# Kernel tuning notes

Hardware: AMD Instinct MI355X
Metric: run time of the kernel (lower is better)

Reference implementation:

```python
import jax, jax.numpy as jnp
import numpy as np

EPS = 1e-12  # torch F.normalize default eps

def l2norm(x, axis):
    n = jnp.sqrt(jnp.sum(x * x, axis=axis, keepdims=True))
    return x / jnp.maximum(n, EPS)

def conv2d(x, w, b, pad):
    y = jax.lax.conv_general_dilated(x, w, (1, 1), [(pad, pad), (pad, pad)],
                                     dimension_numbers=('NCHW', 'OIHW', 'NCHW'))
    return y + b[None, :, None, None]

def setup_inputs() -> dict:
    key = jax.random.key(0)
    ks = jax.random.split(key, 12)
    N, C, H, W, K = 16, 256, 64, 64, 32
    s = 0.05
    return {
        'feature':   jax.random.normal(ks[0], (N, C, H, W), jnp.float32),
        'conv_up_w': jax.random.normal(ks[1], (K, C, 3, 3), jnp.float32) * s,
        'conv_up_b': jax.random.normal(ks[2], (K,), jnp.float32) * s,
        'centroids': jax.random.uniform(ks[3], (K, C), jnp.float32),
        'upfc_w':    jax.random.normal(ks[4], (C, K * C), jnp.float32) * s,
        'upfc_b':    jax.random.normal(ks[5], (C,), jnp.float32) * s,
        't1_w':      jax.random.normal(ks[6], (C, 2 * C, 1, 1), jnp.float32) * s,
        't1_b':      jax.random.normal(ks[7], (C,), jnp.float32) * s,
        't2_w':      jax.random.normal(ks[8], (C, C, 1, 1), jnp.float32) * s,
        't2_b':      jax.random.normal(ks[9], (C,), jnp.float32) * s,
    }

def reference(feature, conv_up_w, conv_up_b, centroids, upfc_w, upfc_b, t1_w, t1_b, t2_w, t2_b):
    N, C, H, W = feature.shape
    K = centroids.shape[0]
    # --- UP branch ---
    xn = l2norm(feature, axis=1)                       # (N,C,H,W)
    sa = jax.nn.softmax(conv2d(xn, conv_up_w, conv_up_b, 1), axis=1)  # (N,K,H,W)
    sa_flat = sa.reshape(N, K, H * W)                  # (N,K,L)
    x_flat = xn.reshape(N, C, H * W)                   # (N,C,L)
    # sum_l sa[n,k,l] * (x[n,c,l] - centroid[k,c])  ==  two matmuls, no (N,K,C,L) tensor
    up = jnp.einsum('nkl,ncl->nkc', sa_flat, x_flat) \
         - jnp.sum(sa_flat, axis=-1)[:, :, None] * centroids[None]   # (N,K,C)
    up = l2norm(up, axis=2).reshape(N, K * C)
    up = l2norm(up, axis=1)
    up = up @ upfc_w.T + upfc_b                        # (N,C)
    up_map = jnp.broadcast_to(up[:, :, None, None], (N, C, H, W))
    # --- transform ---
    nf = jnp.concatenate([feature, up_map], axis=1)    # (N,2C,H,W)
    h = jax.nn.relu(conv2d(nf, t1_w, t1_b, 0))
    return jax.nn.relu(conv2d(h, t2_w, t2_b, 0))
```

## Files before the change

### kernel.cpp

```cpp
#include <hip/hip_runtime.h>
#include <cstdint>

#define N_ 16
#define C_ 256
#define H_ 64
#define W_ 64
#define L_ 4096
#define K_ 32
#define CL_ (C_*L_)
#define KL_ (K_*L_)
#define KC_ (K_*C_)

typedef __attribute__((ext_vector_type(8))) short short8;
typedef __attribute__((ext_vector_type(4))) float f32x4;

__device__ __forceinline__ unsigned short f2bf(float x) {
    unsigned int u = __float_as_uint(x);
    u += 0x7fffu + ((u >> 16) & 1u);
    return (unsigned short)(u >> 16);
}
__device__ __forceinline__ unsigned int pack2(float a, float b) {
    return (unsigned int)f2bf(a) | ((unsigned int)f2bf(b) << 16);
}

__global__ __launch_bounds__(256) void k_prep(
    const float* __restrict__ f, float* __restrict__ rinv,
    unsigned short* __restrict__ xnb)
{
    __shared__ float tile[256 * 34];
    __shared__ float ssred[8 * 33];
    __shared__ float rbuf[32];
    int bid = blockIdx.x;
    int n = bid >> 7;
    int l0 = (bid & 127) << 5;
    int tid = threadIdx.x;
    int l = tid & 31, cb = tid >> 5;
    const float* fp = f + (size_t)n * CL_ + l0 + l;
    float ss = 0.f;
#pragma unroll
    for (int i = 0; i < 32; ++i) {
        int c = (cb << 5) + i;
        float v = fp[(size_t)c * L_];
        tile[c * 34 + l] = v;
        ss = fmaf(v, v, ss);
    }
    ssred[cb * 33 + l] = ss;
    __syncthreads();
    if (tid < 32) {
        float s = 0.f;
#pragma unroll
        for (int j = 0; j < 8; ++j) s += ssred[j * 33 + tid];
        float ri = 1.0f / fmaxf(sqrtf(s), 1e-12f);
        rinv[n * L_ + l0 + tid] = ri;
        rbuf[tid] = ri;
    }
    __syncthreads();
    float ri = rbuf[l];
    unsigned short* op = xnb + ((size_t)n * L_ + l0 + l) * C_ + (cb << 5);
#pragma unroll
    for (int g = 0; g < 4; ++g) {
        unsigned int pk[4];
#pragma unroll
        for (int d = 0; d < 4; ++d) {
            int c = (cb << 5) + (g << 3) + (d << 1);
            pk[d] = pack2(tile[c * 34 + l] * ri, tile[(c + 1) * 34 + l] * ri);
        }
        *(uint4*)(op + (g << 3)) = make_uint4(pk[0], pk[1], pk[2], pk[3]);
    }
}

__global__ __launch_bounds__(256) void k_wpack(const float* __restrict__ w, unsigned short* __restrict__ wb) {
    int i = blockIdx.x * 256 + threadIdx.x;
    int j = i & 7;
    int k = (i >> 3) & 31;
    int q = (i >> 8) & 3;
    int ch = (i >> 10) & 7;
    int t = i >> 13;
    int c = (ch << 5) + (q << 3) + j;
    wb[i] = f2bf(w[k * 2304 + c * 9 + t]);
}

__global__ __launch_bounds__(256) void k_wpack2(const float* __restrict__ w, int stride,
                                                unsigned short* __restrict__ wb) {
    int i = blockIdx.x * 256 + threadIdx.x;
    int co = i >> 8, ci = i & 255;
    wb[i] = f2bf(w[(size_t)co * stride + ci]);
}

__global__ __launch_bounds__(128, 2) void k_conv(
    const unsigned short* __restrict__ xnb, const unsigned short* __restrict__ wb,
    const float* __restrict__ bias, float* __restrict__ sa, float* __restrict__ ssum)
{
    __shared__ __align__(16) unsigned short lsB[2][3 * 34 * 40];
    __shared__ float sred[2][32];
    int bid = blockIdx.x;
    int n = bid & 15, y = (bid >> 4) & 63, px_b = bid >> 10;
    int tid = threadIdx.x;
    int wv = tid >> 6, lane = tid & 63;
    int r = lane & 15, quad = lane >> 4;
    int pxw = (wv << 4) + r;
    int xbase = (px_b << 5) - 1;
    const unsigned short* xb = xnb + (size_t)n * CL_;

    const unsigned short* sptr[4];
    int sidx[4];
    bool svalid[4];
    int scnt = (tid < 24) ? 4 : 3;
#pragma unroll
    for (int k = 0; k < 4; ++k) {
        int j = tid + (k << 7);
        int row = j / 136; if (row > 2) row = 2;
        int rem = j - row * 136;
        int px = rem >> 2, q = rem & 3;
        int yy = y + row - 1, xx = xbase + px;
        bool ok = ((unsigned)yy < 64u) && ((unsigned)xx < 64u);
        int yc = ok ? yy : 0, xc = ok ? xx : 0;
        sptr[k] = xb + (((size_t)(yc << 6) + xc) << 8) + (q << 3);
        svalid[k] = ok;
        sidx[k] = (row * 34 + px) * 40 + (q << 3);
    }
    const uint4 z4 = make_uint4(0, 0, 0, 0);
    uint4 pre[4];
#pragma unroll
    for (int k = 0; k < 4; ++k)
        pre[k] = (k < scnt && svalid[k]) ? *(const uint4*)sptr[k] : z4;

    const unsigned short* wlane = wb + (quad << 8) + (r << 3);

    f32x4 acc0 = (f32x4){0.f, 0.f, 0.f, 0.f};
    f32x4 acc1 = (f32x4){0.f, 0.f, 0.f, 0.f};
    for (int i = 0; i < 8; ++i) {
        int c0 = i << 5;
        unsigned short* buf = lsB[i & 1];
#pragma unroll
        for (int k = 0; k < 4; ++k)
            if (k < scnt) *(uint4*)(buf + sidx[k]) = pre[k];
        __syncthreads();
        if (i < 7) {
#pragma unroll
            for (int k = 0; k < 4; ++k)
                pre[k] = (k < scnt && svalid[k]) ? *(const uint4*)(sptr[k] + c0 + 32) : z4;
        }
#pragma unroll
        for (int dy = 0; dy < 3; ++dy) {
            short8 A0r[3], A1r[3], Br[3];
#pragma unroll
            for (int dx = 0; dx < 3; ++dx) {
                int t = dy * 3 + dx;
                const unsigned short* wp = wlane + (((t << 3) + i) << 10);
                A0r[dx] = *(const short8*)wp;
                A1r[dx] = *(const short8*)(wp + 128);
                Br[dx]  = *(const short8*)(buf + (dy * 34 + pxw + dx) * 40 + (quad << 3));
            }
#pragma unroll
            for (int dx = 0; dx < 3; ++dx) {
                acc0 = __builtin_amdgcn_mfma_f32_16x16x32_bf16(A0r[dx], Br[dx], acc0, 0, 0, 0);
                acc1 = __builtin_amdgcn_mfma_f32_16x16x32_bf16(A1r[dx], Br[dx], acc1, 0, 0, 0);
            }
        }
    }
    float4 b0 = *(const float4*)(bias + (quad << 2));
    float4 b1 = *(const float4*)(bias + 16 + (quad << 2));
    float v[8];
    v[0] = acc0[0] + b0.x; v[1] = acc0[1] + b0.y; v[2] = acc0[2] + b0.z; v[3] = acc0[3] + b0.w;
    v[4] = acc1[0] + b1.x; v[5] = acc1[1] + b1.y; v[6] = acc1[2] + b1.z; v[7] = acc1[3] + b1.w;
    float mx = v[0];
#pragma unroll
    for (int j = 1; j < 8; ++j) mx = fmaxf(mx, v[j]);
    mx = fmaxf(mx, __shfl_xor(mx, 16));
    mx = fmaxf(mx, __shfl_xor(mx, 32));
    float s = 0.f;
#pragma unroll
    for (int j = 0; j < 8; ++j) { v[j] = __expf(v[j] - mx); s += v[j]; }
    s += __shfl_xor(s, 16);
    s += __shfl_xor(s, 32);
    float rs = 1.0f / s;
    float sv8[8];
#pragma unroll
    for (int j = 0; j < 8; ++j) sv8[j] = v[j] * rs;
    int l = (y << 6) + (px_b << 5) + pxw;
    float* sp = sa + (size_t)n * KL_ + l;
#pragma unroll
    for (int j = 0; j < 4; ++j) {
        sp[(size_t)((quad << 2) + j) * L_] = sv8[j];
        sp[(size_t)(16 + (quad << 2) + j) * L_] = sv8[4 + j];
    }
#pragma unroll
    for (int j = 0; j < 8; ++j) {
        float a = sv8[j];
        a += __shfl_xor(a, 1); a += __shfl_xor(a, 2);
        a += __shfl_xor(a, 4); a += __shfl_xor(a, 8);
        sv8[j] = a;
    }
    if (r == 0) {
#pragma unroll
        for (int j = 0; j < 4; ++j) {
            sred[wv][(quad << 2) + j] = sv8[j];
            sred[wv][16 + (quad << 2) + j] = sv8[4 + j];
        }
    }
    __syncthreads();
    if (tid < 32) {
        float t = sred[0][tid] + sred[1][tid];
        atomicAdd(ssum + n * K_ + tid, t);
    }
}

__global__ __launch_bounds__(256) void k_einsum(
    const float* __restrict__ f, const float* __restrict__ rinv,
    const float* __restrict__ sa, float* __restrict__ up)
{
    __shared__ float xn_s[C_ * 33];
    __shared__ float sa_s[K_ * 32];
    int bid = blockIdx.x;
    int n = bid >> 5;
    int l0 = (bid & 31) << 7;
    int tid = threadIdx.x;
    int kq = tid >> 5, cq = tid & 31;
    float acc[4][8];
#pragma unroll
    for (int i = 0; i < 4; ++i)
#pragma unroll
        for (int j = 0; j < 8; ++j) acc[i][j] = 0.f;

    for (int ch = 0; ch < 4; ++ch) {
        int lc = l0 + (ch << 5);
        __syncthreads();
        {
            int crow = tid >> 3, lq = (tid & 7) << 2;
#pragma unroll
            for (int p = 0; p < 8; ++p) {
                int c = (p << 5) + crow;
                float4 f4 = *(const float4*)(f + (size_t)n * CL_ + (size_t)c * L_ + lc + lq);
                float4 r4 = *(const float4*)(rinv + n * L_ + lc + lq);
                float* d = xn_s + c * 33 + lq;
                d[0] = f4.x * r4.x; d[1] = f4.y * r4.y; d[2] = f4.z * r4.z; d[3] = f4.w * r4.w;
            }
        }
        {
            int k = tid >> 3, lq = (tid & 7) << 2;
            float4 a4 = *(const float4*)(sa + (size_t)n * KL_ + (size_t)k * L_ + lc + lq);
            *(float4*)(sa_s + (k << 5) + lq) = a4;
        }
        __syncthreads();
#pragma unroll 4
        for (int l = 0; l < 32; ++l) {
            float sv[4], xv[8];
#pragma unroll
            for (int i = 0; i < 4; ++i) sv[i] = sa_s[((kq << 2) + i) * 32 + l];
#pragma unroll
            for (int j = 0; j < 8; ++j) xv[j] = xn_s[(cq + (j << 5)) * 33 + l];
#pragma unroll
            for (int i = 0; i < 4; ++i)
#pragma unroll
                for (int j = 0; j < 8; ++j) acc[i][j] = fmaf(sv[i], xv[j], acc[i][j]);
        }
    }
    float* upp = up + (size_t)n * KC_;
#pragma unroll
    for (int i = 0; i < 4; ++i)
#pragma unroll
        for (int j = 0; j < 8; ++j)
            atomicAdd(upp + ((kq << 2) + i) * C_ + cq + (j << 5), acc[i][j]);
}

__global__ __launch_bounds__(256) void k_rowfix(
    const float* __restrict__ up, const float* __restrict__ ssum,
    const float* __restrict__ cent, float* __restrict__ upn, float* __restrict__ rowss)
{
    __shared__ float red[256];
    int bid = blockIdx.x;
    int k = bid & 31;
    float sv = ssum[bid];
    float v = up[(size_t)bid * C_ + threadIdx.x] - sv * cent[k * C_ + threadIdx.x];
    red[threadIdx.x] = v * v; __syncthreads();
    for (int st = 128; st > 0; st >>= 1) {
        if (threadIdx.x < st) red[threadIdx.x] += red[threadIdx.x + st];
        __syncthreads();
    }
    float ss = red[0];
    float ri = 1.0f / fmaxf(sqrtf(ss), 1e-12f);
    upn[(size_t)bid * C_ + threadIdx.x] = v * ri;
    if (threadIdx.x == 0) rowss[bid] = ss * ri * ri;
}

__global__ __launch_bounds__(256) void k_fc(
    const float* __restrict__ upn, const float* __restrict__ rowss,
    const float* __restrict__ w, const float* __restrict__ b,
    float* __restrict__ upvec)
{
    __shared__ float rnb[16];
    __shared__ float red[16][5];
    int c = blockIdx.x;
    int tid = threadIdx.x;
    int wv = tid >> 6, lane = tid & 63;
    if (tid < 16) {
        float ts = 0.f;
#pragma unroll
        for (int k = 0; k < K_; ++k) ts += rowss[(tid << 5) + k];
        rnb[tid] = 1.0f / fmaxf(sqrtf(ts), 1e-12f);
    }
    float acc[16];
#pragma unroll
    for (int n = 0; n < 16; ++n) acc[n] = 0.f;
    const float* wr = w + (size_t)c * KC_;
#pragma unroll
    for (int g = 0; g < 8; ++g) {
        int kc = (g << 10) + (tid << 2);
        float4 w4 = *(const float4*)(wr + kc);
#pragma unroll
        for (int n = 0; n < 16; ++n) {
            float4 u4 = *(const float4*)(upn + n * KC_ + kc);
            acc[n] += w4.x * u4.x + w4.y * u4.y + w4.z * u4.z + w4.w * u4.w;
        }
    }
#pragma unroll
    for (int n = 0; n < 16; ++n) {
        float a = acc[n];
#pragma unroll
        for (int s = 1; s < 64; s <<= 1) a += __shfl_xor(a, s);
        if (lane == 0) red[n][wv] = a;
    }
    __syncthreads();
    if (tid < 16) {
        float v = red[tid][0] + red[tid][1] + red[tid][2] + red[tid][3];
        upvec[tid * C_ + c] = v * rnb[tid] + b[c];
    }
}

__global__ __launch_bounds__(256) void k_t1up(
    const float* __restrict__ upvec, const float* __restrict__ t1w,
    const float* __restrict__ t1b, float* __restrict__ t1up)
{
    __shared__ float wld[256];
    int co = blockIdx.x;
    int tid = threadIdx.x;
    wld[tid] = t1w[(size_t)co * 512 + 256 + tid];
    __syncthreads();
    int n = tid >> 4, s = tid & 15;
    float a = 0.f;
#pragma unroll
    for (int i = 0; i < 16; ++i)
        a += wld[s + (i << 4)] * upvec[n * C_ + s + (i << 4)];
#pragma unroll
    for (int st = 1; st < 16; st <<= 1) a += __shfl_xor(a, st);
    if (s == 0) t1up[n * C_ + co] = a + t1b[co];
}

__global__ __launch_bounds__(256) void k_gemm1(
    const float* __restrict__ f, const unsigned short* __restrict__ wb,
    const float* __restrict__ t1up, unsigned short* __restrict__ hb)
{
    __shared__ __align__(16) unsigned int lsB[2][128 * 20];
    int bid = blockIdx.x;
    int co_b = bid & 1, px_b = (bid >> 1) & 31, n = bid >> 6;
    int l0 = px_b << 7;
    int tid = threadIdx.x;
    int wv = tid >> 6, lane = tid & 63;
    int r = lane & 15, quad = lane >> 4;
    int pxl = (wv >> 1) << 6;
    int co0 = (co_b << 7) + ((wv & 1) << 6);
    const float* fb_ = f + (size_t)n * CL_ + l0;
    int c2 = tid & 15, pxg = tid >> 4;

    unsigned int pk[2][4];
#pragma unroll
    for (int k2 = 0; k2 < 2; ++k2) {
        const float* s0 = fb_ + (size_t)(c2 << 1) * L_ + ((pxg + (k2 << 4)) << 2);
        float4 a = *(const float4*)s0;
        float4 b = *(const float4*)(s0 + L_);
        pk[k2][0] = pack2(a.x, b.x); pk[k2][1] = pack2(a.y, b.y);
        pk[k2][2] = pack2(a.z, b.z); pk[k2][3] = pack2(a.w, b.w);
    }
    f32x4 acc[4][4];
#pragma unroll
    for (int i = 0; i < 4; ++i)
#pragma unroll
        for (int j = 0; j < 4; ++j) acc[i][j] = (f32x4){0.f, 0.f, 0.f, 0.f};

    for (int i = 0; i < 8; ++i) {
        int c0 = i << 5;
        unsigned int* buf = lsB[i & 1];
#pragma unroll
        for (int k2 = 0; k2 < 2; ++k2) {
            int base = (pxg + (k2 << 4)) * 80 + c2;
            buf[base]      = pk[k2][0];
            buf[base + 20] = pk[k2][1];
            buf[base + 40] = pk[k2][2];
            buf[base + 60] = pk[k2][3];
        }
        __syncthreads();
        if (i < 7) {
#pragma unroll
            for (int k2 = 0; k2 < 2; ++k2) {
                const float* s0 = fb_ + (size_t)(c0 + 32 + (c2 << 1)) * L_ + ((pxg + (k2 << 4)) << 2);
                float4 a = *(const float4*)s0;
                float4 b = *(const float4*)(s0 + L_);
                pk[k2][0] = pack2(a.x, b.x); pk[k2][1] = pack2(a.y, b.y);
                pk[k2][2] = pack2(a.z, b.z); pk[k2][3] = pack2(a.w, b.w);
            }
        }
        short8 A[4], B[4];
#pragma unroll
        for (int t = 0; t < 4; ++t)
            A[t] = *(const short8*)(wb + (size_t)(co0 + (t << 4) + r) * C_ + c0 + (quad << 3));
#pragma unroll
        for (int t = 0; t < 4; ++t)
            B[t] = *(const short8*)((const unsigned short*)buf + (pxl + (t << 4) + r) * 40 + (quad << 3));
#pragma unroll
        for (int pxt = 0; pxt < 4; ++pxt)
#pragma unroll
            for (int cot = 0; cot < 4; ++cot)
                acc[pxt][cot] = __builtin_amdgcn_mfma_f32_16x16x32_bf16(A[cot], B[pxt], acc[pxt][cot], 0, 0, 0);
    }
#pragma unroll
    for (int pxt = 0; pxt < 4; ++pxt) {
        int px = l0 + pxl + (pxt << 4) + r;
        unsigned short* orow = hb + ((size_t)n * L_ + px) * C_;
#pragma unroll
        for (int cot = 0; cot < 4; ++cot) {
            int cb = co0 + (cot << 4) + (quad << 2);
            float4 bb = *(const float4*)(t1up + n * C_ + cb);
            unsigned int p0 = pack2(fmaxf(acc[pxt][cot][0] + bb.x, 0.f),
                                    fmaxf(acc[pxt][cot][1] + bb.y, 0.f));
            unsigned int p1 = pack2(fmaxf(acc[pxt][cot][2] + bb.z, 0.f),
                                    fmaxf(acc[pxt][cot][3] + bb.w, 0.f));
            *(uint2*)(orow + cb) = make_uint2(p0, p1);
        }
    }
}

__global__ __launch_bounds__(256) void k_gemm2(
    const unsigned short* __restrict__ hb, const unsigned short* __restrict__ wb,
    const float* __restrict__ t2b, float* __restrict__ out)
{
    __shared__ __align__(16) unsigned short lsB[2][128 * 40];
    int bid = blockIdx.x;
    int co_b = bid & 1, px_b = (bid >> 1) & 31, n = bid >> 6;
    int l0 = px_b << 7;
    int tid = threadIdx.x;
    int wv = tid >> 6, lane = tid & 63;
    int r = lane & 15, quad = lane >> 4;
    int pxl = (wv >> 1) << 6;
    int co0 = (co_b << 7) + ((wv & 1) << 6);
    const unsigned short* hrow = hb + ((size_t)n * L_ + l0) * C_;
    int q = tid & 3, pxs = tid >> 2;

    uint4 pre[2];
#pragma unroll
    for (int k2 = 0; k2 < 2; ++k2)
        pre[k2] = *(const uint4*)(hrow + (size_t)(pxs + (k2 << 6)) * C_ + (q << 3));

    f32x4 acc[4][4];
#pragma unroll
    for (int i = 0; i < 4; ++i)
#pragma unroll
        for (int j = 0; j < 4; ++j) acc[i][j] = (f32x4){0.f, 0.f, 0.f, 0.f};

    for (int i = 0; i < 8; ++i) {
        int c0 = i << 5;
        unsigned short* buf = lsB[i & 1];
#pragma unroll
        for (int k2 = 0; k2 < 2; ++k2)
            *(uint4*)(buf + (pxs + (k2 << 6)) * 40 + (q << 3)) = pre[k2];
        __syncthreads();
        if (i < 7) {
#pragma unroll
            for (int k2 = 0; k2 < 2; ++k2)
                pre[k2] = *(const uint4*)(hrow + (size_t)(pxs + (k2 << 6)) * C_ + c0 + 32 + (q << 3));
        }
        short8 A[4], B[4];
#pragma unroll
        for (int t = 0; t < 4; ++t)
            A[t] = *(const short8*)(wb + (size_t)(co0 + (t << 4) + r) * C_ + c0 + (quad << 3));
#pragma unroll
        for (int t = 0; t < 4; ++t)
            B[t] = *(const short8*)(buf + (pxl + (t << 4) + r) * 40 + (quad << 3));
#pragma unroll
        for (int pxt = 0; pxt < 4; ++pxt)
#pragma unroll
            for (int cot = 0; cot < 4; ++cot)
                acc[pxt][cot] = __builtin_amdgcn_mfma_f32_16x16x32_bf16(A[cot], B[pxt], acc[pxt][cot], 0, 0, 0);
    }
#pragma unroll
    for (int pxt = 0; pxt < 4; ++pxt) {
        int px = l0 + pxl + (pxt << 4) + r;
#pragma unroll
        for (int cot = 0; cot < 4; ++cot) {
            int cb = co0 + (cot << 4) + (quad << 2);
            float4 bb = *(const float4*)(t2b + cb);
            out[((size_t)n * C_ + cb + 0) * L_ + px] = fmaxf(acc[pxt][cot][0] + bb.x, 0.f);
            out[((size_t)n * C_ + cb + 1) * L_ + px] = fmaxf(acc[pxt][cot][1] + bb.y, 0.f);
            out[((size_t)n * C_ + cb + 2) * L_ + px] = fmaxf(acc[pxt][cot][2] + bb.z, 0.f);
            out[((size_t)n * C_ + cb + 3) * L_ + px] = fmaxf(acc[pxt][cot][3] + bb.w, 0.f);
        }
    }
}

extern "C" void kernel_launch(void* const* d_in, const int* in_sizes, int n_in,
                              void* d_out, int out_size, void* d_ws, size_t ws_size,
                              hipStream_t stream)
{
    const float* feature = (const float*)d_in[0];
    const float* conv_w  = (const float*)d_in[1];
    const float* conv_b  = (const float*)d_in[2];
    const float* cent    = (const float*)d_in[3];
    const float* upfc_w  = (const float*)d_in[4];
    const float* upfc_b  = (const float*)d_in[5];
    const float* t1w     = (const float*)d_in[6];
    const float* t1b     = (const float*)d_in[7];
    const float* t2w     = (const float*)d_in[8];
    const float* t2b     = (const float*)d_in[9];

    float* ws = (float*)d_ws;
    unsigned short* xnb = (unsigned short*)ws;
    unsigned short* hb  = xnb;
    float* rest  = ws + 8388608;
    float* rinv  = rest;
    float* sa    = rinv + 65536;
    float* up    = sa + 2097152;
    float* ssum  = up + 131072;
    float* upn   = ssum + 512;
    float* rowss = upn + 131072;
    float* upvec = rowss + 512;
    float* t1up  = upvec + 4096;
    unsigned short* wbconv = (unsigned short*)upn;
    unsigned short* t1wb = (unsigned short*)sa;
    unsigned short* t2wb = t1wb + 65536;
    float* out = (float*)d_out;

    hipMemsetAsync(up, 0, (131072 + 512) * sizeof(float), stream);
    k_prep     <<<2048, 256, 0, stream>>>(feature, rinv, xnb);
    k_wpack    <<<288,  256, 0, stream>>>(conv_w, wbconv);
    k_conv     <<<2048, 128, 0, stream>>>(xnb, wbconv, conv_b, sa, ssum);
    k_einsum   <<<512,  256, 0, stream>>>(feature, rinv, sa, up);
    k_rowfix   <<<512,  256, 0, stream>>>(up, ssum, cent, upn, rowss);
    k_wpack2   <<<256,  256, 0, stream>>>(t1w, 512, t1wb);
    k_wpack2   <<<256,  256, 0, stream>>>(t2w, 256, t2wb);
    k_fc       <<<256,  256, 0, stream>>>(upn, rowss, upfc_w, upfc_b, upvec);
    k_t1up     <<<256,  256, 0, stream>>>(upvec, t1w, t1b, t1up);
    k_gemm1    <<<1024, 256, 0, stream>>>(feature, t1wb, t1up, hb);
    k_gemm2    <<<1024, 256, 0, stream>>>(hb, t2wb, t2b, out);
}
```

Before: 337.0 us.

## Stage conv input and weights into LDS via direct global-to-LDS loads

The 3x3 conv kernel now uses global_load_lds to copy input halo tiles and weight slices straight into double-buffered shared memory, replacing register-staged input copies and per-lane global weight reads. Out-of-bounds halo pixels read from a zeroed pad buffer, and the input LDS layout is rearranged to a quad-major order without padding. The aim is to cut VGPR pressure and global-latency stalls in the MFMA loop. In exchange it uses more LDS per block, which may lower occupancy, adds a full vmcnt(0) wait each iteration, and the unpadded layout may cause LDS bank conflicts.

```diff
diff --git a/kernel.cpp b/kernel.cpp
--- a/kernel.cpp
+++ b/kernel.cpp
@@ -23,6 +23,12 @@
     return (unsigned int)f2bf(a) | ((unsigned int)f2bf(b) << 16);
 }
 
+__device__ __forceinline__ void glds16(const void* g, void* l) {
+    __builtin_amdgcn_global_load_lds(
+        (const __attribute__((address_space(1))) unsigned int*)g,
+        (__attribute__((address_space(3))) unsigned int*)l, 16, 0, 0);
+}
+
 __global__ __launch_bounds__(256) void k_prep(
     const float* __restrict__ f, float* __restrict__ rinv,
     unsigned short* __restrict__ xnb)
@@ -89,9 +95,11 @@
 
 __global__ __launch_bounds__(128, 2) void k_conv(
     const unsigned short* __restrict__ xnb, const unsigned short* __restrict__ wb,
-    const float* __restrict__ bias, float* __restrict__ sa, float* __restrict__ ssum)
-{
-    __shared__ __align__(16) unsigned short lsB[2][3 * 34 * 40];
+    const float* __restrict__ bias, const float* __restrict__ zpad,
+    float* __restrict__ sa, float* __restrict__ ssum)
+{
+    __shared__ __align__(16) unsigned short lsB[2][408 * 8];
+    __shared__ __align__(16) unsigned short lsW[2][1152 * 8];
     __shared__ float sred[2][32];
     int bid = blockIdx.x;
     int n = bid & 15, y = (bid >> 4) & 63, px_b = bid >> 10;
@@ -101,61 +109,70 @@
     int pxw = (wv << 4) + r;
     int xbase = (px_b << 5) - 1;
     const unsigned short* xb = xnb + (size_t)n * CL_;
-
-    const unsigned short* sptr[4];
-    int sidx[4];
-    bool svalid[4];
-    int scnt = (tid < 24) ? 4 : 3;
+    const unsigned short* zp = (const unsigned short*)zpad;
+
+    const unsigned short* bsrc[4];
+    bool bact[4];
 #pragma unroll
     for (int k = 0; k < 4; ++k) {
-        int j = tid + (k << 7);
-        int row = j / 136; if (row > 2) row = 2;
-        int rem = j - row * 136;
-        int px = rem >> 2, q = rem & 3;
+        int c = (wv << 6) + (k << 7) + lane;
+        bool act = c < 408;
+        int cc = act ? c : 0;
+        int row = cc / 136;
+        int rem = cc - row * 136;
+        int q = rem / 34;
+        int px = rem - q * 34;
         int yy = y + row - 1, xx = xbase + px;
-        bool ok = ((unsigned)yy < 64u) && ((unsigned)xx < 64u);
-        int yc = ok ? yy : 0, xc = ok ? xx : 0;
-        sptr[k] = xb + (((size_t)(yc << 6) + xc) << 8) + (q << 3);
-        svalid[k] = ok;
-        sidx[k] = (row * 34 + px) * 40 + (q << 3);
-    }
-    const uint4 z4 = make_uint4(0, 0, 0, 0);
-    uint4 pre[4];
-#pragma unroll
-    for (int k = 0; k < 4; ++k)
-        pre[k] = (k < scnt && svalid[k]) ? *(const uint4*)sptr[k] : z4;
-
-    const unsigned short* wlane = wb + (quad << 8) + (r << 3);
+        bool ok = act && ((unsigned)yy < 64u) && ((unsigned)xx < 64u);
+        bsrc[k] = ok ? (xb + (((size_t)(yy << 6) + xx) << 8) + (q << 3)) : zp;
+        bact[k] = act;
+    }
 
     f32x4 acc0 = (f32x4){0.f, 0.f, 0.f, 0.f};
     f32x4 acc1 = (f32x4){0.f, 0.f, 0.f, 0.f};
+
+    {
+#pragma unroll
+        for (int k = 0; k < 4; ++k)
+            if (bact[k]) glds16(bsrc[k], lsB[0] + (((wv << 6) + (k << 7)) << 3));
+#pragma unroll
+        for (int k = 0; k < 9; ++k) {
+            int idx = wv * 9 + k;
+            int t = idx >> 1, h = idx & 1;
+            glds16(wb + (t << 13) + (h << 9) + (lane << 3), lsW[0] + (idx << 9));
+        }
+    }
+
     for (int i = 0; i < 8; ++i) {
-        int c0 = i << 5;
-        unsigned short* buf = lsB[i & 1];
-#pragma unroll
-        for (int k = 0; k < 4; ++k)
-            if (k < scnt) *(uint4*)(buf + sidx[k]) = pre[k];
+        asm volatile("s_waitcnt vmcnt(0)" ::: "memory");
         __syncthreads();
         if (i < 7) {
+            int c1 = (i + 1) << 5;
+            unsigned short* dB = lsB[(i + 1) & 1];
+            unsigned short* dW = lsW[(i + 1) & 1];
 #pragma unroll
             for (int k = 0; k < 4; ++k)
-                pre[k] = (k < scnt && svalid[k]) ? *(const uint4*)(sptr[k] + c0 + 32) : z4;
-        }
+                if (bact[k]) glds16(bsrc[k] + c1, dB + (((wv << 6) + (k << 7)) << 3));
+#pragma unroll
+            for (int k = 0; k < 9; ++k) {
+                int idx = wv * 9 + k;
+                int t = idx >> 1, h = idx & 1;
+                glds16(wb + (t << 13) + (h << 9) + ((i + 1) << 10) + (lane << 3),
+                       dW + (idx << 9));
+            }
+        }
+        const unsigned short* bufB = lsB[i & 1];
+        const unsigned short* bufW = lsW[i & 1];
 #pragma unroll
         for (int dy = 0; dy < 3; ++dy) {
-            short8 A0r[3], A1r[3], Br[3];
 #pragma unroll
             for (int dx = 0; dx < 3; ++dx) {
                 int t = dy * 3 + dx;
-                const unsigned short* wp = wlane + (((t << 3) + i) << 10);
-                A0r[dx] = *(const short8*)wp;
-                A1r[dx] = *(const short8*)(wp + 128);
-                Br[dx]  = *(const short8*)(buf + (dy * 34 + pxw + dx) * 40 + (quad << 3));
-            }
-#pragma unroll
-            for (int dx = 0; dx < 3; ++dx) {
-                acc0 = __builtin_amdgcn_mfma_f32_16x16x32_bf16(A0r[dx], Br[dx], acc0, 0, 0, 0);
-                acc1 = __builtin_amdgcn_mfma_f32_16x16x32_bf16(A1r[dx], Br[dx], acc1, 0, 0, 0);
+                short8 B  = *(const short8*)(bufB + ((((dy << 2) + quad) * 34 + (pxw + dx)) << 3));
+                short8 A0 = *(const short8*)(bufW + (((t << 7) + (quad << 5) + r) << 3));
+                short8 A1 = *(const short8*)(bufW + (((t << 7) + (quad << 5) + 16 + r) << 3));
+                acc0 = __builtin_amdgcn_mfma_f32_16x16x32_bf16(A0, B, acc0, 0, 0, 0);
+                acc1 = __builtin_amdgcn_mfma_f32_16x16x32_bf16(A1, B, acc1, 0, 0, 0);
             }
         }
     }
@@ -520,7 +537,8 @@
     float* sa    = rinv + 65536;
     float* up    = sa + 2097152;
     float* ssum  = up + 131072;
-    float* upn   = ssum + 512;
+    float* zpad  = ssum + 512;
+    float* upn   = zpad + 512;
     float* rowss = upn + 131072;
     float* upvec = rowss + 512;
     float* t1up  = upvec + 4096;
@@ -529,10 +547,10 @@
     unsigned short* t2wb = t1wb + 65536;
     float* out = (float*)d_out;
 
-    hipMemsetAsync(up, 0, (131072 + 512) * sizeof(float), stream);
+    hipMemsetAsync(up, 0, (131072 + 512 + 512) * sizeof(float), stream);
     k_prep     <<<2048, 256, 0, stream>>>(feature, rinv, xnb);
     k_wpack    <<<288,  256, 0, stream>>>(conv_w, wbconv);
-    k_conv     <<<2048, 128, 0, stream>>>(xnb, wbconv, conv_b, sa, ssum);
+    k_conv     <<<2048, 128, 0, stream>>>(xnb, wbconv, conv_b, zpad, sa, ssum);
     k_einsum   <<<512,  256, 0, stream>>>(feature, rinv, sa, up);
     k_rowfix   <<<512,  256, 0, stream>>>(up, ssum, cent, upn, rowss);
     k_wpack2   <<<256,  256, 0, stream>>>(t1w, 512, t1wb);
```

New measurement: 310.7 us. -7.8%, faster.
